# Kernel tuning notes

Hardware: AMD Instinct MI355X
Metric: run time of the kernel (lower is better)

The kernel has to match this reference:

```python
import jax, jax.numpy as jnp
import numpy as np

EPS = 1e-5  # torch BatchNorm1d default eps
NH, KD, D_V = 8, 64, 128  # num_heads, key_dim, per-head value dim (attn_ratio*key_dim)


def hardswish(x):
    return x * jnp.clip(x + 3.0, 0.0, 6.0) / 6.0


def linear_bn(x, W, g, b):
    # Linear (no bias) followed by BatchNorm1d in training mode: batch stats
    # over all leading dims (torch flattens (B,N) before BN).
    y = x @ W.T
    yf = y.reshape(-1, y.shape[-1])
    mu = yf.mean(0)
    var = yf.var(0)  # biased variance, matching BN normalization
    return (y - mu) * (g / jnp.sqrt(var + EPS)) + b


def setup_inputs() -> dict:
    key = jax.random.key(0)
    ks = jax.random.split(key, 22)
    B, C, H, W, NT, D = 8, 1024, 96, 96, 60, 512
    dh = NH * D_V          # 1024
    h_kv = dh + NH * KD    # 1536
    hf = 2 * D             # 1024 (mr=2)

    def p(k, shape, s=0.02):
        return jax.random.normal(k, shape, jnp.float32) * s

    return {
        "im_emd": jax.random.normal(ks[0], (B, C, H, W), jnp.float32),
        "text_emd": jax.random.normal(ks[1], (NT, D), jnp.float32),
        "W_dc": p(ks[2], (D, C)), "g_dc": 1.0 + p(ks[3], (D,)), "b_dc": p(ks[4], (D,)),
        "W_kv": p(ks[5], (h_kv, D)), "g_kv": 1.0 + p(ks[6], (h_kv,)), "b_kv": p(ks[7], (h_kv,)),
        "W_q": p(ks[8], (NH * KD, D)), "g_q": 1.0 + p(ks[9], (NH * KD,)), "b_q": p(ks[10], (NH * KD,)),
        "W_proj": p(ks[11], (D, dh)), "g_proj": 1.0 + p(ks[12], (D,)), "b_proj": p(ks[13], (D,)),
        "biases": p(ks[14], (NH, 10000)),  # relative-position bias table (100x100 offsets)
        "W_f1": p(ks[15], (hf, D)), "g_f1": 1.0 + p(ks[16], (hf,)), "b_f1": p(ks[17], (hf,)),
        "W_f2": p(ks[18], (D, hf)), "g_f2": 1.0 + p(ks[19], (D,)), "b_f2": p(ks[20], (D,)),
    }


def _bias_idx(NT, H, W):
    # Offset table built row-major over product(range(100), range(100)) =>
    # attention_offsets[(a,b)] == 100*a + b. Text token t maps to grid point
    # (t//100, t%100); image token n to (n//W, n%W).
    t = np.arange(NT)
    n = np.arange(H * W)
    dx = np.abs(t[:, None] // 100 - n[None, :] // W)
    dy = np.abs(t[:, None] % 100 - n[None, :] % W)
    return 100 * dx + dy  # [NT, N]


def reference(im_emd, text_emd, W_dc, g_dc, b_dc, W_kv, g_kv, b_kv,
              W_q, g_q, b_q, W_proj, g_proj, b_proj, biases,
              W_f1, g_f1, b_f1, W_f2, g_f2, b_f2):
    B, C, H, W = im_emd.shape
    N = H * W
    NT, D = text_emd.shape
    dh = NH * D_V
    scale = KD ** -0.5

    # image tokens -> embed_dim
    x = im_emd.reshape(B, C, N).transpose(0, 2, 1)          # [B,N,C]
    xd = hardswish(linear_bn(x, W_dc, g_dc, b_dc))          # [B,N,D]

    # Attentioninv: text queries attend over image keys/values
    kv = linear_bn(xd, W_kv, g_kv, b_kv).reshape(B, N, NH, KD + D_V)
    k, v = kv[..., :KD], kv[..., KD:]                       # [B,N,h,64], [B,N,h,128]
    q = linear_bn(text_emd[None], W_q, g_q, b_q).reshape(NT, NH, KD)  # [NT,h,64]

    idx = jnp.asarray(_bias_idx(NT, H, W))                  # [NT,N] static
    bias = biases[:, idx]                                   # [h,NT,N] gather

    attn = jnp.einsum('thd,bnhd->bhtn', q, k) * scale + bias[None]
    attn = jax.nn.softmax(attn, axis=-1)                    # [B,h,NT,N]
    out = jnp.einsum('bhtn,bnhd->bthd', attn, v).reshape(B, NT, dh)
    out = linear_bn(hardswish(out), W_proj, g_proj, b_proj)  # [B,NT,D]

    textd = text_emd[None] + out                            # residual (broadcast)

    # ffntext: Linear_BN -> Hardswish -> Linear_BN(bn_weight_init=0) + residual
    f = hardswish(linear_bn(textd, W_f1, g_f1, b_f1))
    f = linear_bn(f, W_f2, g_f2, b_f2)
    textd = f + textd
    return textd[0]  # [NT, D]
```

## Files before the change

### kernel.cpp

```cpp
#include <hip/hip_runtime.h>
#include <hip/hip_bf16.h>
#include <stdint.h>

typedef short bf16x8 __attribute__((ext_vector_type(8)));
typedef float f32x4 __attribute__((ext_vector_type(4)));

__device__ __forceinline__ float b2f(ushort u){ return __uint_as_float(((uint32_t)u)<<16); }
__device__ __forceinline__ ushort f2b(float f){
  uint32_t u = __float_as_uint(f);
  u += 0x7fffu + ((u>>16)&1u);
  return (ushort)(u>>16);
}
__device__ __forceinline__ float hswish(float x){ return x*fminf(fmaxf(x+3.f,0.f),6.f)*(1.f/6.f); }

__device__ __forceinline__ void gll16(const void* g, void* l){
  __builtin_amdgcn_global_load_lds((const __attribute__((address_space(1))) void*)g,
                                   (__attribute__((address_space(3))) void*)l, 16, 0, 0);
}

__global__ void zero_f32(float* __restrict__ p, int n){
  int i = blockIdx.x*256 + threadIdx.x;
  if (i < n) p[i] = 0.f;
}

__global__ void cvt_bf16(const float* __restrict__ in, ushort* __restrict__ out, int n){
  int i = blockIdx.x*256 + threadIdx.x;
  if (i < n) out[i] = f2b(in[i]);
}

__global__ __launch_bounds__(256) void transpose_kernel(const float* __restrict__ im, ushort* __restrict__ At){
  __shared__ float tb[64][65];
  const int b = blockIdx.z, c0 = blockIdx.y*64, n0 = blockIdx.x*64;
  const int tid = threadIdx.x;
  const int cl = tid >> 2, q = tid & 3;
  #pragma unroll
  for (int it=0; it<4; ++it){
    int nn = q*4 + it*16;
    float4 v = *(const float4*)&im[((size_t)(b*1024 + c0 + cl))*9216 + n0 + nn];
    tb[cl][nn+0]=v.x; tb[cl][nn+1]=v.y; tb[cl][nn+2]=v.z; tb[cl][nn+3]=v.w;
  }
  __syncthreads();
  const int nr = tid >> 4, c4 = (tid & 15)*4;
  #pragma unroll
  for (int ps=0; ps<4; ++ps){
    int nn = nr + ps*16;
    ushort4 u;
    u.x = f2b(tb[c4+0][nn]); u.y = f2b(tb[c4+1][nn]);
    u.z = f2b(tb[c4+2][nn]); u.w = f2b(tb[c4+3][nn]);
    *(ushort4*)&At[((size_t)(b*9216 + n0 + nn))*1024 + c0 + c4] = u;
  }
}

__global__ __launch_bounds__(256) void gemm_bt(
    const ushort* __restrict__ A, const ushort* __restrict__ Bm,
    ushort* __restrict__ Cm, float* __restrict__ sums, float* __restrict__ sqs,
    int NT, int N, int K)
{
  __shared__ __align__(16) ushort As[128*64];
  __shared__ __align__(16) ushort Bs[128*64];
  const int tid = threadIdx.x;
  const int l = tid & 63;
  const int w = tid >> 6;
  const int wm = w >> 1, wn = w & 1;
  const int chunk = gridDim.x >> 3;
  const int wg = (blockIdx.x & 7)*chunk + (blockIdx.x >> 3);
  const int tn = wg % NT, tm = wg / NT;
  const size_t n0 = (size_t)tn * 128;
  const size_t m0 = (size_t)tm * 128;
  const int lr = l & 15, lk = l >> 4;
  const int wbase = tid & ~63;

  f32x4 acc[4][4];
  #pragma unroll
  for (int i=0;i<4;++i)
    #pragma unroll
    for (int j=0;j<4;++j) acc[i][j] = (f32x4){0.f,0.f,0.f,0.f};

  for (int kt = 0; kt < K; kt += 64) {
    #pragma unroll
    for (int it=0; it<4; ++it) {
      int idx = it*256 + tid;
      int row = idx >> 3, c8 = idx & 7;
      int sc8 = c8 ^ (row & 7);
      gll16(&A[(m0+row)*K + kt + sc8*8], &As[(it*256 + wbase)*8]);
      gll16(&Bm[(n0+row)*K + kt + sc8*8], &Bs[(it*256 + wbase)*8]);
    }
    __syncthreads();
    #pragma unroll
    for (int kk=0; kk<64; kk+=32) {
      bf16x8 af[4], bfr[4];
      #pragma unroll
      for (int i=0;i<4;++i){
        int row = wm*64 + i*16 + lr;
        af[i] = *(const bf16x8*)&As[row*64 + ((kk + lk*8) ^ ((row&7)<<3))];
      }
      #pragma unroll
      for (int j=0;j<4;++j){
        int row = wn*64 + j*16 + lr;
        bfr[j] = *(const bf16x8*)&Bs[row*64 + ((kk + lk*8) ^ ((row&7)<<3))];
      }
      #pragma unroll
      for (int i=0;i<4;++i)
        #pragma unroll
        for (int j=0;j<4;++j)
          acc[i][j] = __builtin_amdgcn_mfma_f32_16x16x32_bf16(af[i], bfr[j], acc[i][j], 0, 0, 0);
    }
    __syncthreads();
  }
  #pragma unroll
  for (int i=0;i<4;++i)
    #pragma unroll
    for (int j=0;j<4;++j)
      #pragma unroll
      for (int r=0;r<4;++r) {
        size_t row = m0 + wm*64 + i*16 + lk*4 + r;
        size_t col = n0 + wn*64 + j*16 + lr;
        Cm[row*N + col] = f2b(acc[i][j][r]);
      }
  #pragma unroll
  for (int j=0;j<4;++j){
    float cs=0.f, cq=0.f;
    #pragma unroll
    for (int i=0;i<4;++i)
      #pragma unroll
      for (int r=0;r<4;++r){ float v=acc[i][j][r]; cs+=v; cq+=v*v; }
    cs += __shfl_xor(cs,16); cs += __shfl_xor(cs,32);
    cq += __shfl_xor(cq,16); cq += __shfl_xor(cq,32);
    if (lk==0){
      int col = (int)n0 + wn*64 + j*16 + lr;
      atomicAdd(&sums[col], cs);
      atomicAdd(&sqs [col], cq);
    }
  }
}

__global__ void bn_finalize(const float* __restrict__ sums, const float* __restrict__ sqs,
                            const float* __restrict__ g, const float* __restrict__ bb,
                            float* __restrict__ scale, float* __restrict__ shift, int C, float invn)
{
  int c = blockIdx.x*256 + threadIdx.x;
  if (c < C){
    float mu = sums[c]*invn;
    float var = sqs[c]*invn - mu*mu;
    float k = g[c] * rsqrtf(var + 1e-5f);
    scale[c] = k;
    shift[c] = bb[c] - mu*k;
  }
}

__global__ __launch_bounds__(256) void bn_hswish(ushort* __restrict__ y, const float* __restrict__ scale, const float* __restrict__ shift)
{
  __shared__ float sc[512], sh[512];
  for (int i=threadIdx.x;i<512;i+=256){ sc[i]=scale[i]; sh[i]=shift[i]; }
  __syncthreads();
  const size_t total = (size_t)73728*512/8;
  for (size_t idx = (size_t)blockIdx.x*256+threadIdx.x; idx < total; idx += (size_t)gridDim.x*256){
    uint4 u = *(uint4*)&y[idx*8];
    ushort* up = (ushort*)&u;
    int c0 = ((int)(idx & 63))*8;
    #pragma unroll
    for (int e=0;e<8;++e){
      float x = b2f(up[e])*sc[c0+e] + sh[c0+e];
      up[e] = f2b(hswish(x));
    }
    *(uint4*)&y[idx*8] = u;
  }
}

__global__ __launch_bounds__(256) void q_gemm(const float* __restrict__ text, const float* __restrict__ Wq, float* __restrict__ qraw)
{
  __shared__ __align__(16) float xr[512];
  const int t = blockIdx.x, tid = threadIdx.x;
  for (int i=tid;i<512;i+=256) xr[i] = text[t*512+i];
  __syncthreads();
  #pragma unroll
  for (int cj=0;cj<2;++cj){
    int c = cj*256+tid;
    const float4* wp = (const float4*)(Wq + (size_t)c*512);
    const float4* xp = (const float4*)xr;
    float a=0.f;
    for (int u=0;u<128;++u){
      float4 wv = wp[u], xv = xp[u];
      a += wv.x*xv.x + wv.y*xv.y + wv.z*xv.z + wv.w*xv.w;
    }
    qraw[t*512+c]=a;
  }
}

__global__ __launch_bounds__(512) void q_bn_qh(const float* __restrict__ qraw, const float* __restrict__ g,
                                               const float* __restrict__ bb,
                                               const float* __restrict__ scale2, const float* __restrict__ shift2,
                                               ushort* __restrict__ Qh, float* __restrict__ cQ)
{
  const int c = threadIdx.x;
  const int h = c >> 6, d = c & 63;
  float s=0.f,q=0.f;
  for (int t=0;t<60;++t){ float v = qraw[t*512+c]; s+=v; q+=v*v; }
  float mu=s*(1.f/60.f), var=q*(1.f/60.f)-mu*mu;
  float k = g[c]*rsqrtf(var+1e-5f);
  float sh = bb[c]-mu*k;
  const float sk = scale2[h*192+d]*0.125f;
  const float tk = shift2[h*192+d]*0.125f;
  for (int t=0;t<60;++t){
    float qv = qraw[t*512+c]*k+sh;
    Qh[(h*64+t)*64+d] = f2b(qv*sk);
    float contrib = qv*tk;
    #pragma unroll
    for (int o=32;o>0;o>>=1) contrib += __shfl_xor(contrib,o);
    if (d==0) cQ[h*64+t] = contrib;
  }
  for (int t=60;t<64;++t) Qh[(h*64+t)*64+d] = 0;
  if (d==0) for (int t=60;t<64;++t) cQ[h*64+t] = 0.f;
}

__global__ __launch_bounds__(256) void attn_flash(
    const ushort* __restrict__ Qh, const float* __restrict__ cQ,
    const ushort* __restrict__ kv, const float* __restrict__ biases,
    float* __restrict__ Op, float* __restrict__ Mp, float* __restrict__ Lp)
{
  __shared__ __align__(16) ushort Qs[64*72];
  __shared__ __align__(16) ushort vt[128*68];
  __shared__ __align__(16) ushort Pw[4][16*72];
  __shared__ float bias_l[1200];
  __shared__ float cQs[64];
  const int tid = threadIdx.x;
  const int l = tid & 63, w = tid >> 6;
  const int lr = l & 15, lk = l >> 4;
  const int nc = blockIdx.x, h = blockIdx.y, b = blockIdx.z;
  const int bh = b*8+h;
  for (int cid = tid; cid < 512; cid += 256){
    int row = cid >> 3, c8 = cid & 7;
    *(uint4*)&Qs[row*72 + c8*8] = *(const uint4*)&Qh[(size_t)(h*64+row)*64 + c8*8];
  }
  for (int i = tid; i < 1200; i += 256) bias_l[i] = biases[h*10000 + nc*1200 + i];
  if (tid < 64) cQs[tid] = cQ[h*64 + tid];

  float m_run[4] = {-1e30f,-1e30f,-1e30f,-1e30f};
  float l_run[4] = {0.f,0.f,0.f,0.f};
  f32x4 acc_o[8];
  #pragma unroll
  for (int j=0;j<8;++j) acc_o[j] = (f32x4){0.f,0.f,0.f,0.f};
  __syncthreads();

  for (int tile=0; tile<18; ++tile){
    const int n0 = nc*1152 + tile*64;
    if (tile) __syncthreads();
    #pragma unroll
    for (int c2=0;c2<4;++c2){
      int cid = c2*256 + tid;
      int row = cid >> 4, dv0 = (cid & 15)*8;
      uint4 vv = *(const uint4*)&kv[((size_t)(b*9216 + n0 + row))*1536 + h*192 + 64 + dv0];
      const ushort* vb8 = (const ushort*)&vv;
      #pragma unroll
      for (int e=0;e<8;++e) vt[(dv0+e)*68 + row] = vb8[e];
    }
    __syncthreads();
    f32x4 sa[4];
    #pragma unroll
    for (int j=0;j<4;++j) sa[j]=(f32x4){0.f,0.f,0.f,0.f};
    const ushort* kbase = kv + ((size_t)(b*9216 + n0))*1536 + h*192;
    #pragma unroll
    for (int kk=0; kk<64; kk+=32){
      bf16x8 af = *(const bf16x8*)&Qs[(w*16+lr)*72 + kk + lk*8];
      #pragma unroll
      for (int j=0;j<4;++j){
        bf16x8 bf_ = *(const bf16x8*)&kbase[(size_t)(j*16+lr)*1536 + kk + lk*8];
        sa[j] = __builtin_amdgcn_mfma_f32_16x16x32_bf16(af, bf_, sa[j], 0,0,0);
      }
    }
    float mt[4] = {-1e30f,-1e30f,-1e30f,-1e30f};
    #pragma unroll
    for (int j=0;j<4;++j){
      int n = n0 + j*16 + lr;
      int py = n/96;
      int px = n - py*96;
      int pyl = py - nc*12;
      #pragma unroll
      for (int r=0;r<4;++r){
        int t = w*16 + lk*4 + r;
        int dd = t - px; dd = dd<0?-dd:dd;
        float s = sa[j][r] + cQs[t] + bias_l[pyl*100 + dd];
        sa[j][r] = s;
        mt[r] = fmaxf(mt[r], s);
      }
    }
    #pragma unroll
    for (int r=0;r<4;++r){
      #pragma unroll
      for (int o=1;o<16;o<<=1) mt[r] = fmaxf(mt[r], __shfl_xor(mt[r], o));
      float mnew = fmaxf(m_run[r], mt[r]);
      float ef = __expf(m_run[r] - mnew);
      m_run[r] = mnew;
      l_run[r] *= ef;
      #pragma unroll
      for (int j2=0;j2<8;++j2) acc_o[j2][r] *= ef;
    }
    float rs[4] = {0.f,0.f,0.f,0.f};
    #pragma unroll
    for (int j=0;j<4;++j)
      #pragma unroll
      for (int r=0;r<4;++r){
        float pe = __expf(sa[j][r] - m_run[r]);
        rs[r] += pe;
        Pw[w][(lk*4+r)*72 + j*16 + lr] = f2b(pe);
      }
    #pragma unroll
    for (int r=0;r<4;++r){
      #pragma unroll
      for (int o=1;o<16;o<<=1) rs[r] += __shfl_xor(rs[r], o);
      l_run[r] += rs[r];
    }
    #pragma unroll
    for (int kk=0; kk<64; kk+=32){
      bf16x8 pa = *(const bf16x8*)&Pw[w][lr*72 + kk + lk*8];
      #pragma unroll
      for (int j2=0;j2<8;++j2){
        const ushort* vp = &vt[(j2*16+lr)*68 + kk + lk*8];
        uint2 a0 = *(const uint2*)vp, a1 = *(const uint2*)(vp+4);
        struct PP { uint2 a,b; } pp{a0,a1};
        bf16x8 vb = __builtin_bit_cast(bf16x8, pp);
        acc_o[j2] = __builtin_amdgcn_mfma_f32_16x16x32_bf16(pa, vb, acc_o[j2], 0,0,0);
      }
    }
  }
  float* ob = Op + (((size_t)nc*64 + bh)*64)*128;
  #pragma unroll
  for (int j2=0;j2<8;++j2)
    #pragma unroll
    for (int r=0;r<4;++r){
      int row = w*16 + lk*4 + r;
      ob[(size_t)row*128 + j2*16 + lr] = acc_o[j2][r];
    }
  if (lr == 0){
    #pragma unroll
    for (int r=0;r<4;++r){
      int row = w*16 + lk*4 + r;
      Mp[(nc*64+bh)*64 + row] = m_run[r];
      Lp[(nc*64+bh)*64 + row] = l_run[r];
    }
  }
}

__global__ __launch_bounds__(128) void attn_combine(
    const float* __restrict__ Op, const float* __restrict__ Mp, const float* __restrict__ Lp,
    float* __restrict__ attn_o)
{
  const int t = blockIdx.x, bh = blockIdx.y;
  const int b = bh >> 3, h = bh & 7;
  const int dv = threadIdx.x;
  float mv[8];
  float m_g = -1e30f;
  #pragma unroll
  for (int i=0;i<8;++i){ mv[i] = Mp[(i*64+bh)*64 + t]; m_g = fmaxf(m_g, mv[i]); }
  float lsum = 0.f;
  #pragma unroll
  for (int i=0;i<8;++i) lsum += Lp[(i*64+bh)*64 + t] * __expf(mv[i]-m_g);
  float o = 0.f;
  #pragma unroll
  for (int i=0;i<8;++i)
    o += Op[(((size_t)i*64 + bh)*64 + t)*128 + dv] * __expf(mv[i]-m_g);
  attn_o[(size_t)(b*60+t)*1024 + h*128 + dv] = o / lsum;
}

template<int CIN, int COUT, int MODE>
__global__ __launch_bounds__(256) void rowgemm8(
    const float* __restrict__ X, const float* __restrict__ Wt,
    const float* __restrict__ sc, const float* __restrict__ sh,
    float* __restrict__ out)
{
  __shared__ __align__(16) float xr[8][CIN];
  const int rb0 = blockIdx.x*8, tid = threadIdx.x;
  for (int i=tid; i<8*CIN; i+=256){
    int rr = i / CIN, cc = i % CIN;
    float v = X[(size_t)(rb0+rr)*CIN + cc];
    if constexpr (MODE==2) v = v*sc[cc]+sh[cc];
    if constexpr (MODE==3){ int idx = 64 + (cc&127) + (cc>>7)*192; v = v*sc[idx]+sh[idx]; }
    if constexpr (MODE>=1) v = hswish(v);
    xr[rr][cc]=v;
  }
  __syncthreads();
  int c = blockIdx.y*256 + tid;
  const float4* wp = (const float4*)(Wt + (size_t)c*CIN);
  float a[8] = {0.f,0.f,0.f,0.f,0.f,0.f,0.f,0.f};
  for (int u=0;u<CIN/4;++u){
    float4 wv = wp[u];
    #pragma unroll
    for (int rr=0;rr<8;++rr){
      float4 xv = *(const float4*)&xr[rr][u*4];
      a[rr] += wv.x*xv.x + wv.y*xv.y + wv.z*xv.z + wv.w*xv.w;
    }
  }
  #pragma unroll
  for (int rr=0;rr<8;++rr) out[(size_t)(rb0+rr)*COUT + c] = a[rr];
}

template<int C>
__global__ void stats480(const float* __restrict__ X, const float* __restrict__ g,
                         const float* __restrict__ bb, float* __restrict__ sc, float* __restrict__ sh)
{
  int c = blockIdx.x*256 + threadIdx.x;
  float s=0.f, q=0.f;
  for (int r=0;r<480;++r){ float v = X[(size_t)r*C + c]; s+=v; q+=v*v; }
  float mu = s*(1.f/480.f), var = q*(1.f/480.f)-mu*mu;
  float k = g[c] * rsqrtf(var+1e-5f);
  sc[c]=k; sh[c]=bb[c] - mu*k;
}

__global__ void make_textd(const float* __restrict__ praw, const float* __restrict__ sp, const float* __restrict__ tp,
                           const float* __restrict__ text, float* __restrict__ textd)
{
  int i = blockIdx.x*256+threadIdx.x;
  if (i < 480*512){
    int c = i & 511, rb = i >> 9, t = rb % 60;
    textd[i] = text[t*512+c] + praw[i]*sp[c]+tp[c];
  }
}

__global__ void final_out(const float* __restrict__ f2raw, const float* __restrict__ sf, const float* __restrict__ tf,
                          const float* __restrict__ textd, float* __restrict__ outp)
{
  int i = blockIdx.x*256+threadIdx.x;
  if (i < 60*512){ int c = i & 511; outp[i] = f2raw[i]*sf[c]+tf[c] + textd[i]; }
}

extern "C" void kernel_launch(void* const* d_in, const int* in_sizes, int n_in,
                              void* d_out, int out_size, void* d_ws, size_t ws_size,
                              hipStream_t stream)
{
  (void)in_sizes; (void)n_in; (void)out_size; (void)ws_size;
  const float* im    = (const float*)d_in[0];
  const float* text  = (const float*)d_in[1];
  const float* W_dc  = (const float*)d_in[2];
  const float* g_dc  = (const float*)d_in[3];
  const float* b_dc  = (const float*)d_in[4];
  const float* W_kv  = (const float*)d_in[5];
  const float* g_kv  = (const float*)d_in[6];
  const float* b_kv  = (const float*)d_in[7];
  const float* W_q   = (const float*)d_in[8];
  const float* g_q   = (const float*)d_in[9];
  const float* b_q   = (const float*)d_in[10];
  const float* W_proj= (const float*)d_in[11];
  const float* g_proj= (const float*)d_in[12];
  const float* b_proj= (const float*)d_in[13];
  const float* biases= (const float*)d_in[14];
  const float* W_f1  = (const float*)d_in[15];
  const float* g_f1  = (const float*)d_in[16];
  const float* b_f1  = (const float*)d_in[17];
  const float* W_f2  = (const float*)d_in[18];
  const float* g_f2  = (const float*)d_in[19];
  const float* b_f2  = (const float*)d_in[20];
  float* outp = (float*)d_out;

  char* p = (char*)d_ws;
  auto alloc = [&](size_t bytes)->char*{ char* r = p; p += (bytes+255)&~(size_t)255; return r; };
  float* s1_sum = (float*)alloc(512*4);
  float* s1_sq  = (float*)alloc(512*4);
  float* s2_sum = (float*)alloc(1536*4);
  float* s2_sq  = (float*)alloc(1536*4);
  float* zero_base = s1_sum; const int zero_n = 4096;
  float* attn_o = (float*)alloc((size_t)480*1024*4);
  float* sc1 = (float*)alloc(512*4);
  float* sh1 = (float*)alloc(512*4);
  float* sc2 = (float*)alloc(1536*4);
  float* sh2 = (float*)alloc(1536*4);
  float* qraw = (float*)alloc(60*512*4);
  ushort* Qh = (ushort*)alloc((size_t)8*64*64*2);
  float* cQ = (float*)alloc(512*4);
  float* proj_raw = (float*)alloc((size_t)480*512*4);
  float* sp=(float*)alloc(512*4); float* tp=(float*)alloc(512*4);
  float* textd=(float*)alloc((size_t)480*512*4);
  float* sf1=(float*)alloc(1024*4); float* tf1=(float*)alloc(1024*4);
  float* f1_raw=(float*)alloc((size_t)480*1024*4);
  float* sf2=(float*)alloc(512*4); float* tf2=(float*)alloc(512*4);
  float* f2_raw=(float*)alloc((size_t)480*512*4);
  float* Op = (float*)alloc((size_t)8*64*64*128*4);
  float* Mp = (float*)alloc((size_t)8*64*64*4);
  float* Lp = (float*)alloc((size_t)8*64*64*4);
  ushort* Wdc_b = (ushort*)alloc((size_t)512*1024*2);
  ushort* Wkv_b = (ushort*)alloc((size_t)1536*512*2);
  ushort* y1 = (ushort*)alloc((size_t)73728*512*2);
  ushort* kv = (ushort*)alloc((size_t)73728*1536*2);
  ushort* At = (ushort*)alloc((size_t)73728*1024*2);

  zero_f32<<<16,256,0,stream>>>(zero_base, zero_n);
  cvt_bf16<<<2048,256,0,stream>>>(W_dc, Wdc_b, 512*1024);
  cvt_bf16<<<3072,256,0,stream>>>(W_kv, Wkv_b, 1536*512);
  transpose_kernel<<<dim3(144,16,8),256,0,stream>>>(im, At);
  gemm_bt<<<2304,256,0,stream>>>(At, Wdc_b, y1, s1_sum, s1_sq, 4, 512, 1024);
  bn_finalize<<<2,256,0,stream>>>(s1_sum, s1_sq, g_dc, b_dc, sc1, sh1, 512, 1.f/73728.f);
  bn_hswish<<<2048,256,0,stream>>>(y1, sc1, sh1);
  gemm_bt<<<6912,256,0,stream>>>(y1, Wkv_b, kv, s2_sum, s2_sq, 12, 1536, 512);
  bn_finalize<<<6,256,0,stream>>>(s2_sum, s2_sq, g_kv, b_kv, sc2, sh2, 1536, 1.f/73728.f);
  q_gemm<<<60,256,0,stream>>>(text, W_q, qraw);
  q_bn_qh<<<1,512,0,stream>>>(qraw, g_q, b_q, sc2, sh2, Qh, cQ);
  attn_flash<<<dim3(8,8,8),256,0,stream>>>(Qh, cQ, kv, biases, Op, Mp, Lp);
  attn_combine<<<dim3(60,64),128,0,stream>>>(Op, Mp, Lp, attn_o);
  rowgemm8<1024,512,3><<<dim3(60,2),256,0,stream>>>(attn_o, W_proj, sc2, sh2, proj_raw);
  stats480<512><<<2,256,0,stream>>>(proj_raw, g_proj, b_proj, sp, tp);
  make_textd<<<960,256,0,stream>>>(proj_raw, sp, tp, text, textd);
  rowgemm8<512,1024,0><<<dim3(60,4),256,0,stream>>>(textd, W_f1, nullptr, nullptr, f1_raw);
  stats480<1024><<<4,256,0,stream>>>(f1_raw, g_f1, b_f1, sf1, tf1);
  rowgemm8<1024,512,2><<<dim3(60,2),256,0,stream>>>(f1_raw, W_f2, sf1, tf1, f2_raw);
  stats480<512><<<2,256,0,stream>>>(f2_raw, g_f2, b_f2, sf2, tf2);
  final_out<<<120,256,0,stream>>>(f2_raw, sf2, tf2, textd, outp);
}
```

Measured before the change: 763.5 us.

## Split KV into K and transposed V, fuse small kernels and BN stats

```diff
diff --git a/kernel.cpp b/kernel.cpp
--- a/kernel.cpp
+++ b/kernel.cpp
@@ -18,14 +18,13 @@
                                    (__attribute__((address_space(3))) void*)l, 16, 0, 0);
 }
 
-__global__ void zero_f32(float* __restrict__ p, int n){
+__global__ void init_kernel(const float* __restrict__ Wdc, const float* __restrict__ Wkv,
+                            ushort* __restrict__ Wdc_b, ushort* __restrict__ Wkv_b,
+                            float* __restrict__ zbase){
   int i = blockIdx.x*256 + threadIdx.x;
-  if (i < n) p[i] = 0.f;
-}
-
-__global__ void cvt_bf16(const float* __restrict__ in, ushort* __restrict__ out, int n){
-  int i = blockIdx.x*256 + threadIdx.x;
-  if (i < n) out[i] = f2b(in[i]);
+  if (i < 8192) zbase[i] = 0.f;
+  for (int j=i; j<512*1024; j+=262144) Wdc_b[j] = f2b(Wdc[j]);
+  for (int j=i; j<1536*512; j+=262144) Wkv_b[j] = f2b(Wkv[j]);
 }
 
 __global__ __launch_bounds__(256) void transpose_kernel(const float* __restrict__ im, ushort* __restrict__ At){
@@ -51,9 +50,11 @@
   }
 }
 
+template<int SPLIT>
 __global__ __launch_bounds__(256) void gemm_bt(
     const ushort* __restrict__ A, const ushort* __restrict__ Bm,
-    ushort* __restrict__ Cm, float* __restrict__ sums, float* __restrict__ sqs,
+    ushort* __restrict__ Cm, ushort* __restrict__ Vt,
+    float* __restrict__ sums, float* __restrict__ sqs,
     int NT, int N, int K)
 {
   __shared__ __align__(16) ushort As[128*64];
@@ -107,16 +108,41 @@
     }
     __syncthreads();
   }
-  #pragma unroll
-  for (int i=0;i<4;++i)
-    #pragma unroll
-    for (int j=0;j<4;++j)
-      #pragma unroll
-      for (int r=0;r<4;++r) {
-        size_t row = m0 + wm*64 + i*16 + lk*4 + r;
-        size_t col = n0 + wn*64 + j*16 + lr;
-        Cm[row*N + col] = f2b(acc[i][j][r]);
-      }
+  if constexpr (SPLIT==0){
+    #pragma unroll
+    for (int i=0;i<4;++i)
+      #pragma unroll
+      for (int j=0;j<4;++j)
+        #pragma unroll
+        for (int r=0;r<4;++r) {
+          size_t row = m0 + wm*64 + i*16 + lk*4 + r;
+          size_t col = n0 + wn*64 + j*16 + lr;
+          Cm[row*N + col] = f2b(acc[i][j][r]);
+        }
+  } else {
+    const int bq = (int)(m0/9216);
+    const int nbase = (int)(m0 - (size_t)bq*9216);
+    #pragma unroll
+    for (int j=0;j<4;++j){
+      int c = (int)n0 + wn*64 + j*16 + lr;
+      int h = c/192, rcol = c - h*192;
+      #pragma unroll
+      for (int i=0;i<4;++i){
+        int nrow = nbase + wm*64 + i*16 + lk*4;
+        if (rcol < 64){
+          ushort* kb = Cm + ((size_t)(bq*9216 + nrow))*512 + h*64 + rcol;
+          #pragma unroll
+          for (int r=0;r<4;++r) kb[(size_t)r*512] = f2b(acc[i][j][r]);
+        } else {
+          int dv = rcol - 64;
+          ushort4 u;
+          u.x=f2b(acc[i][j][0]); u.y=f2b(acc[i][j][1]);
+          u.z=f2b(acc[i][j][2]); u.w=f2b(acc[i][j][3]);
+          *(ushort4*)&Vt[((size_t)((bq*8+h)*128 + dv))*9216 + nrow] = u;
+        }
+      }
+    }
+  }
   #pragma unroll
   for (int j=0;j<4;++j){
     float cs=0.f, cq=0.f;
@@ -215,11 +241,12 @@
 
 __global__ __launch_bounds__(256) void attn_flash(
     const ushort* __restrict__ Qh, const float* __restrict__ cQ,
-    const ushort* __restrict__ kv, const float* __restrict__ biases,
+    const ushort* __restrict__ Kbuf, const ushort* __restrict__ Vt,
+    const float* __restrict__ biases,
     float* __restrict__ Op, float* __restrict__ Mp, float* __restrict__ Lp)
 {
   __shared__ __align__(16) ushort Qs[64*72];
-  __shared__ __align__(16) ushort vt[128*68];
+  __shared__ __align__(16) ushort vt[128*64];
   __shared__ __align__(16) ushort Pw[4][16*72];
   __shared__ float bias_l[1200];
   __shared__ float cQs[64];
@@ -228,6 +255,7 @@
   const int lr = l & 15, lk = l >> 4;
   const int nc = blockIdx.x, h = blockIdx.y, b = blockIdx.z;
   const int bh = b*8+h;
+  const int wbase = tid & ~63;
   for (int cid = tid; cid < 512; cid += 256){
     int row = cid >> 3, c8 = cid & 7;
     *(uint4*)&Qs[row*72 + c8*8] = *(const uint4*)&Qh[(size_t)(h*64+row)*64 + c8*8];
@@ -235,6 +263,9 @@
   for (int i = tid; i < 1200; i += 256) bias_l[i] = biases[h*10000 + nc*1200 + i];
   if (tid < 64) cQs[tid] = cQ[h*64 + tid];
 
+  const ushort* vsrc = Vt + (size_t)bh*128*9216;
+  const ushort* kchunk = Kbuf + (size_t)b*9216*512 + h*64;
+
   float m_run[4] = {-1e30f,-1e30f,-1e30f,-1e30f};
   float l_run[4] = {0.f,0.f,0.f,0.f};
   f32x4 acc_o[8];
@@ -246,28 +277,28 @@
     const int n0 = nc*1152 + tile*64;
     if (tile) __syncthreads();
     #pragma unroll
-    for (int c2=0;c2<4;++c2){
-      int cid = c2*256 + tid;
-      int row = cid >> 4, dv0 = (cid & 15)*8;
-      uint4 vv = *(const uint4*)&kv[((size_t)(b*9216 + n0 + row))*1536 + h*192 + 64 + dv0];
-      const ushort* vb8 = (const ushort*)&vv;
-      #pragma unroll
-      for (int e=0;e<8;++e) vt[(dv0+e)*68 + row] = vb8[e];
+    for (int it=0; it<4; ++it){
+      int idx = it*256 + tid;
+      int row = idx >> 3, c8 = idx & 7;
+      int sc8 = c8 ^ (row & 7);
+      gll16(&vsrc[(size_t)row*9216 + n0 + sc8*8], &vt[(it*256 + wbase)*8]);
     }
     __syncthreads();
     f32x4 sa[4];
     #pragma unroll
     for (int j=0;j<4;++j) sa[j]=(f32x4){0.f,0.f,0.f,0.f};
-    const ushort* kbase = kv + ((size_t)(b*9216 + n0))*1536 + h*192;
+    const ushort* kbase = kchunk + (size_t)n0*512;
+    __builtin_amdgcn_s_setprio(1);
     #pragma unroll
     for (int kk=0; kk<64; kk+=32){
       bf16x8 af = *(const bf16x8*)&Qs[(w*16+lr)*72 + kk + lk*8];
       #pragma unroll
       for (int j=0;j<4;++j){
-        bf16x8 bf_ = *(const bf16x8*)&kbase[(size_t)(j*16+lr)*1536 + kk + lk*8];
+        bf16x8 bf_ = *(const bf16x8*)&kbase[(size_t)(j*16+lr)*512 + kk + lk*8];
         sa[j] = __builtin_amdgcn_mfma_f32_16x16x32_bf16(af, bf_, sa[j], 0,0,0);
       }
     }
+    __builtin_amdgcn_s_setprio(0);
     float mt[4] = {-1e30f,-1e30f,-1e30f,-1e30f};
     #pragma unroll
     for (int j=0;j<4;++j){
@@ -310,18 +341,18 @@
       for (int o=1;o<16;o<<=1) rs[r] += __shfl_xor(rs[r], o);
       l_run[r] += rs[r];
     }
+    __builtin_amdgcn_s_setprio(1);
     #pragma unroll
     for (int kk=0; kk<64; kk+=32){
       bf16x8 pa = *(const bf16x8*)&Pw[w][lr*72 + kk + lk*8];
       #pragma unroll
       for (int j2=0;j2<8;++j2){
-        const ushort* vp = &vt[(j2*16+lr)*68 + kk + lk*8];
-        uint2 a0 = *(const uint2*)vp, a1 = *(const uint2*)(vp+4);
-        struct PP { uint2 a,b; } pp{a0,a1};
-        bf16x8 vb = __builtin_bit_cast(bf16x8, pp);
+        int dv = j2*16 + lr;
+        bf16x8 vb = *(const bf16x8*)&vt[dv*64 + ((kk + lk*8) ^ ((dv&7)<<3))];
         acc_o[j2] = __builtin_amdgcn_mfma_f32_16x16x32_bf16(pa, vb, acc_o[j2], 0,0,0);
       }
     }
+    __builtin_amdgcn_s_setprio(0);
   }
   float* ob = Op + (((size_t)nc*64 + bh)*64)*128;
   #pragma unroll
@@ -366,16 +397,21 @@
 __global__ __launch_bounds__(256) void rowgemm8(
     const float* __restrict__ X, const float* __restrict__ Wt,
     const float* __restrict__ sc, const float* __restrict__ sh,
-    float* __restrict__ out)
+    const float* __restrict__ text, float* __restrict__ textd,
+    float* __restrict__ out, float* __restrict__ osum, float* __restrict__ osq)
 {
   __shared__ __align__(16) float xr[8][CIN];
   const int rb0 = blockIdx.x*8, tid = threadIdx.x;
   for (int i=tid; i<8*CIN; i+=256){
     int rr = i / CIN, cc = i % CIN;
     float v = X[(size_t)(rb0+rr)*CIN + cc];
-    if constexpr (MODE==2) v = v*sc[cc]+sh[cc];
-    if constexpr (MODE==3){ int idx = 64 + (cc&127) + (cc>>7)*192; v = v*sc[idx]+sh[idx]; }
-    if constexpr (MODE>=1) v = hswish(v);
+    if constexpr (MODE==2){ v = v*sc[cc]+sh[cc]; v = hswish(v); }
+    if constexpr (MODE==3){ int idx = 64 + (cc&127) + (cc>>7)*192; v = v*sc[idx]+sh[idx]; v = hswish(v); }
+    if constexpr (MODE==4){
+      int t = (rb0+rr) % 60;
+      v = text[t*CIN+cc] + v*sc[cc]+sh[cc];
+      if (blockIdx.y == 0) textd[(size_t)(rb0+rr)*CIN + cc] = v;
+    }
     xr[rr][cc]=v;
   }
   __syncthreads();
@@ -390,30 +426,14 @@
       a[rr] += wv.x*xv.x + wv.y*xv.y + wv.z*xv.z + wv.w*xv.w;
     }
   }
-  #pragma unroll
-  for (int rr=0;rr<8;++rr) out[(size_t)(rb0+rr)*COUT + c] = a[rr];
-}
-
-template<int C>
-__global__ void stats480(const float* __restrict__ X, const float* __restrict__ g,
-                         const float* __restrict__ bb, float* __restrict__ sc, float* __restrict__ sh)
-{
-  int c = blockIdx.x*256 + threadIdx.x;
-  float s=0.f, q=0.f;
-  for (int r=0;r<480;++r){ float v = X[(size_t)r*C + c]; s+=v; q+=v*v; }
-  float mu = s*(1.f/480.f), var = q*(1.f/480.f)-mu*mu;
-  float k = g[c] * rsqrtf(var+1e-5f);
-  sc[c]=k; sh[c]=bb[c] - mu*k;
-}
-
-__global__ void make_textd(const float* __restrict__ praw, const float* __restrict__ sp, const float* __restrict__ tp,
-                           const float* __restrict__ text, float* __restrict__ textd)
-{
-  int i = blockIdx.x*256+threadIdx.x;
-  if (i < 480*512){
-    int c = i & 511, rb = i >> 9, t = rb % 60;
-    textd[i] = text[t*512+c] + praw[i]*sp[c]+tp[c];
-  }
+  float ps=0.f, pq=0.f;
+  #pragma unroll
+  for (int rr=0;rr<8;++rr){
+    out[(size_t)(rb0+rr)*COUT + c] = a[rr];
+    ps += a[rr]; pq += a[rr]*a[rr];
+  }
+  atomicAdd(&osum[c], ps);
+  atomicAdd(&osq [c], pq);
 }
 
 __global__ void final_out(const float* __restrict__ f2raw, const float* __restrict__ sf, const float* __restrict__ tf,
@@ -457,7 +477,13 @@
   float* s1_sq  = (float*)alloc(512*4);
   float* s2_sum = (float*)alloc(1536*4);
   float* s2_sq  = (float*)alloc(1536*4);
-  float* zero_base = s1_sum; const int zero_n = 4096;
+  float* s3_sum = (float*)alloc(512*4);
+  float* s3_sq  = (float*)alloc(512*4);
+  float* s4_sum = (float*)alloc(1024*4);
+  float* s4_sq  = (float*)alloc(1024*4);
+  float* s5_sum = (float*)alloc(512*4);
+  float* s5_sq  = (float*)alloc(512*4);
+  float* zero_base = s1_sum;
   float* attn_o = (float*)alloc((size_t)480*1024*4);
   float* sc1 = (float*)alloc(512*4);
   float* sh1 = (float*)alloc(512*4);
@@ -479,28 +505,26 @@
   ushort* Wdc_b = (ushort*)alloc((size_t)512*1024*2);
   ushort* Wkv_b = (ushort*)alloc((size_t)1536*512*2);
   ushort* y1 = (ushort*)alloc((size_t)73728*512*2);
-  ushort* kv = (ushort*)alloc((size_t)73728*1536*2);
+  ushort* Kbuf = (ushort*)alloc((size_t)73728*512*2);
+  ushort* Vt  = (ushort*)alloc((size_t)64*128*9216*2);
   ushort* At = (ushort*)alloc((size_t)73728*1024*2);
 
-  zero_f32<<<16,256,0,stream>>>(zero_base, zero_n);
-  cvt_bf16<<<2048,256,0,stream>>>(W_dc, Wdc_b, 512*1024);
-  cvt_bf16<<<3072,256,0,stream>>>(W_kv, Wkv_b, 1536*512);
+  init_kernel<<<1024,256,0,stream>>>(W_dc, W_kv, Wdc_b, Wkv_b, zero_base);
   transpose_kernel<<<dim3(144,16,8),256,0,stream>>>(im, At);
-  gemm_bt<<<2304,256,0,stream>>>(At, Wdc_b, y1, s1_sum, s1_sq, 4, 512, 1024);
+  gemm_bt<0><<<2304,256,0,stream>>>(At, Wdc_b, y1, nullptr, s1_sum, s1_sq, 4, 512, 1024);
   bn_finalize<<<2,256,0,stream>>>(s1_sum, s1_sq, g_dc, b_dc, sc1, sh1, 512, 1.f/73728.f);
   bn_hswish<<<2048,256,0,stream>>>(y1, sc1, sh1);
-  gemm_bt<<<6912,256,0,stream>>>(y1, Wkv_b, kv, s2_sum, s2_sq, 12, 1536, 512);
+  gemm_bt<1><<<6912,256,0,stream>>>(y1, Wkv_b, Kbuf, Vt, s2_sum, s2_sq, 12, 1536, 512);
   bn_finalize<<<6,256,0,stream>>>(s2_sum, s2_sq, g_kv, b_kv, sc2, sh2, 1536, 1.f/73728.f);
   q_gemm<<<60,256,0,stream>>>(text, W_q, qraw);
   q_bn_qh<<<1,512,0,stream>>>(qraw, g_q, b_q, sc2, sh2, Qh, cQ);
-  attn_flash<<<dim3(8,8,8),256,0,stream>>>(Qh, cQ, kv, biases, Op, Mp, Lp);
+  attn_flash<<<dim3(8,8,8),256,0,stream>>>(Qh, cQ, Kbuf, Vt, biases, Op, Mp, Lp);
   attn_combine<<<dim3(60,64),128,0,stream>>>(Op, Mp, Lp, attn_o);
-  rowgemm8<1024,512,3><<<dim3(60,2),256,0,stream>>>(attn_o, W_proj, sc2, sh2, proj_raw);
-  stats480<512><<<2,256,0,stream>>>(proj_raw, g_proj, b_proj, sp, tp);
-  make_textd<<<960,256,0,stream>>>(proj_raw, sp, tp, text, textd);
-  rowgemm8<512,1024,0><<<dim3(60,4),256,0,stream>>>(textd, W_f1, nullptr, nullptr, f1_raw);
-  stats480<1024><<<4,256,0,stream>>>(f1_raw, g_f1, b_f1, sf1, tf1);
-  rowgemm8<1024,512,2><<<dim3(60,2),256,0,stream>>>(f1_raw, W_f2, sf1, tf1, f2_raw);
-  stats480<512><<<2,256,0,stream>>>(f2_raw, g_f2, b_f2, sf2, tf2);
+  rowgemm8<1024,512,3><<<dim3(60,2),256,0,stream>>>(attn_o, W_proj, sc2, sh2, nullptr, nullptr, proj_raw, s3_sum, s3_sq);
+  bn_finalize<<<2,256,0,stream>>>(s3_sum, s3_sq, g_proj, b_proj, sp, tp, 512, 1.f/480.f);
+  rowgemm8<512,1024,4><<<dim3(60,4),256,0,stream>>>(proj_raw, W_f1, sp, tp, text, textd, f1_raw, s4_sum, s4_sq);
+  bn_finalize<<<4,256,0,stream>>>(s4_sum, s4_sq, g_f1, b_f1, sf1, tf1, 1024, 1.f/480.f);
+  rowgemm8<1024,512,2><<<dim3(60,2),256,0,stream>>>(f1_raw, W_f2, sf1, tf1, nullptr, nullptr, f2_raw, s5_sum, s5_sq);
+  bn_finalize<<<2,256,0,stream>>>(s5_sum, s5_sq, g_f2, b_f2, sf2, tf2, 512, 1.f/480.f);
   final_out<<<120,256,0,stream>>>(f2_raw, sf2, tf2, textd, outp);
 }
```

New measurement: 747.2 us. 2.1% less time.
